# Performance work log

Measured on AMD Instinct MI355X. Metric: run time of the kernel, lower is better.

The kernel has to match this reference:

```python
import jax, jax.numpy as jnp
import numpy as np

B, S, F = 16, 511, 128           # batch, input seq len, n_features
D, H, NB = 512, 8, 6             # embedding_dim, n_heads, n_blocks
DH = D // H                      # d_head
MLP = 4 * D                      # mlp_ratio=4 hard-coded in FxtBlock
OUT = 1                          # out_d
T = S + 1                        # tokens incl. cls
EPS = 1e-5                       # torch LayerNorm default eps


def pos_emb(seq_len, d):
    # matches get_positional_embeddings: sin for even j, cos for odd j (with j-1 exponent)
    i = np.arange(seq_len, dtype=np.float32)[:, None]
    j = np.arange(d)
    je = np.where(j % 2 == 0, j, j - 1).astype(np.float32)
    ang = i / (10000.0 ** (je / d))
    pe = np.where(j % 2 == 0, np.sin(ang), np.cos(ang))
    return jnp.asarray(pe, jnp.float32)


def layernorm(x, g, b):
    m = jnp.mean(x, axis=-1, keepdims=True)
    v = jnp.mean((x - m) ** 2, axis=-1, keepdims=True)
    return (x - m) * jax.lax.rsqrt(v + EPS) * g + b


def setup_inputs() -> dict:
    key = jax.random.key(0)
    ks = jax.random.split(key, 12)
    g = lambda k, shape: jax.random.normal(k, shape, jnp.float32) * 0.02
    return {
        "src": jax.random.normal(ks[0], (B, S, F), jnp.float32),
        "emb_W": g(ks[1], (F, D)), "emb_b": jnp.zeros((D,), jnp.float32),
        "cls_tok": jax.random.uniform(ks[2], (1, D), jnp.float32),
        "ln1_g": jnp.ones((NB, D), jnp.float32), "ln1_b": jnp.zeros((NB, D), jnp.float32),
        "Wq": g(ks[3], (NB, H, DH, DH)), "bq": jnp.zeros((NB, H, DH), jnp.float32),
        "Wk": g(ks[4], (NB, H, DH, DH)), "bk": jnp.zeros((NB, H, DH), jnp.float32),
        "Wv": g(ks[5], (NB, H, DH, DH)), "bv": jnp.zeros((NB, H, DH), jnp.float32),
        "ln2_g": jnp.ones((NB, D), jnp.float32), "ln2_b": jnp.zeros((NB, D), jnp.float32),
        "W1": g(ks[6], (NB, D, MLP)), "b1": jnp.zeros((NB, MLP), jnp.float32),
        "W2": g(ks[7], (NB, MLP, D)), "b2": jnp.zeros((NB, D), jnp.float32),
        "head_W": g(ks[8], (D, OUT)), "head_b": jnp.zeros((OUT,), jnp.float32),
    }


def reference(src, emb_W, emb_b, cls_tok, ln1_g, ln1_b, Wq, bq, Wk, bk, Wv, bv,
              ln2_g, ln2_b, W1, b1, W2, b2, head_W, head_b):
    b = src.shape[0]
    x = src @ emb_W + emb_b                                    # [B,S,D]
    cls = jnp.broadcast_to(cls_tok[None], (b, 1, D))
    x = jnp.concatenate([cls, x], axis=1) + pos_emb(T, D)[None]  # [B,T,D]
    scale = 1.0 / jnp.sqrt(jnp.float32(DH))
    for i in range(NB):
        h = layernorm(x, ln1_g[i], ln1_b[i])
        hh = h.reshape(b, T, H, DH)
        q = jnp.einsum('bthd,hde->bhte', hh, Wq[i]) + bq[i][None, :, None, :]
        k = jnp.einsum('bthd,hde->bhte', hh, Wk[i]) + bk[i][None, :, None, :]
        v = jnp.einsum('bthd,hde->bhte', hh, Wv[i]) + bv[i][None, :, None, :]
        attn = jax.nn.softmax(jnp.einsum('bhse,bhte->bhst', q, k) * scale, axis=-1)
        o = jnp.einsum('bhst,bhte->bhse', attn, v)             # [B,H,T,DH]
        x = x + o.transpose(0, 2, 1, 3).reshape(b, T, D)
        h2 = layernorm(x, ln2_g[i], ln2_b[i])
        x = x + (jax.nn.gelu(h2 @ W1[i] + b1[i], approximate=False) @ W2[i] + b2[i])
    return jax.nn.sigmoid(x[:, 0] @ head_W + head_b)           # [B,OUT]
```

## Files before the change

### kernel.cpp

```cpp
#include <hip/hip_runtime.h>
#include <hip/hip_bf16.h>
#include <math.h>

#define B 16
#define S 511
#define F 128
#define D 512
#define H 8
#define NB 6
#define DH 64
#define MLPD 2048
#define T 512
#define EPS 1e-5f

typedef unsigned short ushort;
typedef __attribute__((ext_vector_type(8))) short short8;
typedef __attribute__((ext_vector_type(4))) float floatx4;

__device__ __forceinline__ ushort f2bf(float f) {
    union { float f; unsigned u; } cv; cv.f = f;
    unsigned r = (cv.u + 0x7fff + ((cv.u >> 16) & 1)) >> 16;
    return (ushort)r;
}

__device__ __forceinline__ float fast_gelu(float x) {
    float z = fabsf(x) * 0.70710678118f;
    float t = 1.0f / (1.0f + 0.3275911f * z);
    float p = ((((1.061405429f * t - 1.453152027f) * t + 1.421413741f) * t
               - 0.284496736f) * t + 0.254829592f) * t;
    float erfv = 1.0f - p * __expf(-z * z);
    erfv = copysignf(erfv, x);
    return 0.5f * x * (1.0f + erfv);
}

__global__ void castsrc_kernel(const float* __restrict__ src, ushort* __restrict__ srcb) {
    int row = blockIdx.x;
    int t = row & (T - 1), b = row >> 9;
    int tid = threadIdx.x;
    ushort v = 0;
    if (t > 0) v = f2bf(src[((size_t)b * S + (t - 1)) * F + tid]);
    srcb[(size_t)row * F + tid] = v;
}

__global__ void wtrans_kernel(const float* __restrict__ W,
                              ushort* __restrict__ Wt,
                              int K, int N) {
    int kb = blockIdx.x * 32, nb = blockIdx.y * 32, mat = blockIdx.z;
    __shared__ float tile[32][33];
    int tid = threadIdx.x;
    int c = tid & 31, r0 = tid >> 5;
    const float* Wm = W + (size_t)mat * K * N;
    ushort* Wtm = Wt + (size_t)mat * K * N;
    #pragma unroll
    for (int l = 0; l < 4; ++l) {
        int r = r0 + l * 8;
        tile[r][c] = Wm[(size_t)(kb + r) * N + nb + c];
    }
    __syncthreads();
    #pragma unroll
    for (int l = 0; l < 4; ++l) {
        int r = r0 + l * 8;
        Wtm[(size_t)(nb + r) * K + kb + c] = f2bf(tile[c][r]);
    }
}

__global__ void wtransq_kernel(const float* __restrict__ Wq, const float* __restrict__ Wk,
                               const float* __restrict__ Wv,
                               ushort* __restrict__ WqT, ushort* __restrict__ WkT,
                               ushort* __restrict__ WvT) {
    int mat = blockIdx.x;
    int which = blockIdx.y;
    const float* W = (which == 0 ? Wq : which == 1 ? Wk : Wv) + (size_t)mat * 4096;
    ushort* O = (which == 0 ? WqT : which == 1 ? WkT : WvT) + (size_t)mat * 4096;
    __shared__ float t[64][65];
    int tid = threadIdx.x;
    int r0 = tid >> 6, c = tid & 63;
    #pragma unroll
    for (int l = 0; l < 16; ++l) {
        int row = r0 * 16 + l;
        t[row][c] = W[row * 64 + c];
    }
    __syncthreads();
    #pragma unroll
    for (int l = 0; l < 16; ++l) {
        int row = r0 * 16 + l;
        O[row * 64 + c] = f2bf(t[c][row]);
    }
}

__device__ __forceinline__ void gload_lds16(const ushort* g, ushort* l) {
    __builtin_amdgcn_global_load_lds((const __attribute__((address_space(1))) unsigned int*)g,
                                     (__attribute__((address_space(3))) unsigned int*)l,
                                     16, 0, 0);
}

#define S_WAITCNT_VM(N) asm volatile("s_waitcnt vmcnt(" #N ")" ::: "memory")
#define S_WAITCNT_LGKM0 asm volatile("s_waitcnt lgkmcnt(0)" ::: "memory")

__global__ __launch_bounds__(256) void embed_gemm(const ushort* __restrict__ A,
                                                  const ushort* __restrict__ Bt,
                                                  const float* __restrict__ emb_b,
                                                  const float* __restrict__ cls_tok,
                                                  float* __restrict__ x) {
    __shared__ ushort As[64 * 32];
    __shared__ ushort Bs[64 * 32];
    int tid = threadIdx.x;
    int lane = tid & 63;
    int w = __builtin_amdgcn_readfirstlane(tid >> 6);
    int quad = lane >> 4, l15 = lane & 15;
    int wr = (w >> 1) * 32, wc = (w & 1) * 32;
    int m0 = blockIdx.x * 64, n0 = blockIdx.y * 64;

    floatx4 acc[2][2];
    #pragma unroll
    for (int i = 0; i < 2; ++i)
        #pragma unroll
        for (int j = 0; j < 2; ++j) acc[i][j] = (floatx4)0.f;

    int lrow = lane >> 2;
    int lk = (lane & 3) * 8;
    const ushort* Ag = A + (size_t)(m0 + 16 * w + lrow) * F + lk;
    const ushort* Bg = Bt + (size_t)(n0 + 16 * w + lrow) * F + lk;
    ushort* AsW = &As[16 * w * 32];
    ushort* BsW = &Bs[16 * w * 32];
    int fa = l15 * 32 + quad * 8;

    for (int kt = 0; kt < F; kt += 32) {
        gload_lds16(Ag + kt, AsW);
        gload_lds16(Bg + kt, BsW);
        __syncthreads();
        short8 af[2], bf[2];
        #pragma unroll
        for (int i = 0; i < 2; ++i) af[i] = *(const short8*)&As[(wr + 16 * i) * 32 + fa];
        #pragma unroll
        for (int j = 0; j < 2; ++j) bf[j] = *(const short8*)&Bs[(wc + 16 * j) * 32 + fa];
        #pragma unroll
        for (int i = 0; i < 2; ++i)
            #pragma unroll
            for (int j = 0; j < 2; ++j)
                acc[i][j] = __builtin_amdgcn_mfma_f32_16x16x32_bf16(af[i], bf[j], acc[i][j], 0, 0, 0);
        __syncthreads();
    }

    const float LOG1E4 = 9.210340371976184f;
    int rbase = (lane >> 4) * 4;
    int cidx = lane & 15;
    #pragma unroll
    for (int j = 0; j < 2; ++j) {
        int gc = n0 + wc + 16 * j + cidx;
        float je = (float)(gc & ~1);
        float freq = expf(-(je / (float)D) * LOG1E4);
        float ebv = emb_b[gc];
        float clsv = cls_tok[gc];
        bool odd = (gc & 1);
        #pragma unroll
        for (int i = 0; i < 2; ++i) {
            int gr = m0 + wr + 16 * i + rbase;
            #pragma unroll
            for (int reg = 0; reg < 4; ++reg) {
                int row = gr + reg;
                int t = row & (T - 1);
                float ang = (float)t * freq;
                float pe = odd ? cosf(ang) : sinf(ang);
                float val = (t == 0) ? (clsv + pe) : (acc[i][j][reg] + ebv + pe);
                x[(size_t)row * D + gc] = val;
            }
        }
    }
}

__global__ __launch_bounds__(256) void ln_kernel(const float* __restrict__ xin,
                                                 const float* __restrict__ g,
                                                 const float* __restrict__ bb,
                                                 ushort* __restrict__ out) {
    int lane = threadIdx.x & 63;
    int row = blockIdx.x * 4 + (threadIdx.x >> 6);
    const float* xr = xin + (size_t)row * D + lane * 8;
    float4 a0 = *(const float4*)xr;
    float4 a1 = *(const float4*)(xr + 4);
    float s = a0.x + a0.y + a0.z + a0.w + a1.x + a1.y + a1.z + a1.w;
    #pragma unroll
    for (int off = 1; off < 64; off <<= 1) s += __shfl_xor(s, off);
    float mean = s * (1.0f / (float)D);
    float d0 = a0.x - mean, d1 = a0.y - mean, d2 = a0.z - mean, d3 = a0.w - mean;
    float d4 = a1.x - mean, d5 = a1.y - mean, d6 = a1.z - mean, d7 = a1.w - mean;
    float sq = d0*d0 + d1*d1 + d2*d2 + d3*d3 + d4*d4 + d5*d5 + d6*d6 + d7*d7;
    #pragma unroll
    for (int off = 1; off < 64; off <<= 1) sq += __shfl_xor(sq, off);
    float rstd = rsqrtf(sq * (1.0f / (float)D) + EPS);
    const float* gp = g + lane * 8;
    const float* bp = bb + lane * 8;
    float4 g0 = *(const float4*)gp, g1 = *(const float4*)(gp + 4);
    float4 b0 = *(const float4*)bp, b1 = *(const float4*)(bp + 4);
    short8 o;
    o[0] = (short)f2bf(d0 * rstd * g0.x + b0.x);
    o[1] = (short)f2bf(d1 * rstd * g0.y + b0.y);
    o[2] = (short)f2bf(d2 * rstd * g0.z + b0.z);
    o[3] = (short)f2bf(d3 * rstd * g0.w + b0.w);
    o[4] = (short)f2bf(d4 * rstd * g1.x + b1.x);
    o[5] = (short)f2bf(d5 * rstd * g1.y + b1.y);
    o[6] = (short)f2bf(d6 * rstd * g1.z + b1.z);
    o[7] = (short)f2bf(d7 * rstd * g1.w + b1.w);
    *(short8*)(out + (size_t)row * D + lane * 8) = o;
}

__global__ __launch_bounds__(256) void ln_fuse_kernel(float* __restrict__ x,
                                                      const float* __restrict__ p0,
                                                      const float* __restrict__ g,
                                                      const float* __restrict__ bb,
                                                      ushort* __restrict__ out) {
    int lane = threadIdx.x & 63;
    int row = blockIdx.x * 4 + (threadIdx.x >> 6);
    size_t base = (size_t)row * D + lane * 8;
    float* xr = x + base;
    float4 a0 = *(const float4*)xr;
    float4 a1 = *(const float4*)(xr + 4);
    float4 q0 = *(const float4*)(p0 + base);
    float4 q1 = *(const float4*)(p0 + base + 4);
    a0.x += q0.x; a0.y += q0.y; a0.z += q0.z; a0.w += q0.w;
    a1.x += q1.x; a1.y += q1.y; a1.z += q1.z; a1.w += q1.w;
    *(float4*)xr = a0;
    *(float4*)(xr + 4) = a1;
    float s = a0.x + a0.y + a0.z + a0.w + a1.x + a1.y + a1.z + a1.w;
    #pragma unroll
    for (int off = 1; off < 64; off <<= 1) s += __shfl_xor(s, off);
    float mean = s * (1.0f / (float)D);
    float d0 = a0.x - mean, d1 = a0.y - mean, d2 = a0.z - mean, d3 = a0.w - mean;
    float d4 = a1.x - mean, d5 = a1.y - mean, d6 = a1.z - mean, d7 = a1.w - mean;
    float sq = d0*d0 + d1*d1 + d2*d2 + d3*d3 + d4*d4 + d5*d5 + d6*d6 + d7*d7;
    #pragma unroll
    for (int off = 1; off < 64; off <<= 1) sq += __shfl_xor(sq, off);
    float rstd = rsqrtf(sq * (1.0f / (float)D) + EPS);
    const float* gp = g + lane * 8;
    const float* bp = bb + lane * 8;
    float4 g0 = *(const float4*)gp, g1 = *(const float4*)(gp + 4);
    float4 b0 = *(const float4*)bp, b1 = *(const float4*)(bp + 4);
    short8 o;
    o[0] = (short)f2bf(d0 * rstd * g0.x + b0.x);
    o[1] = (short)f2bf(d1 * rstd * g0.y + b0.y);
    o[2] = (short)f2bf(d2 * rstd * g0.z + b0.z);
    o[3] = (short)f2bf(d3 * rstd * g0.w + b0.w);
    o[4] = (short)f2bf(d4 * rstd * g1.x + b1.x);
    o[5] = (short)f2bf(d5 * rstd * g1.y + b1.y);
    o[6] = (short)f2bf(d6 * rstd * g1.z + b1.z);
    o[7] = (short)f2bf(d7 * rstd * g1.w + b1.w);
    *(short8*)(out + (size_t)row * D + lane * 8) = o;
}

__global__ __launch_bounds__(256) void qkv_kernel(
        const ushort* __restrict__ hb,
        const ushort* __restrict__ WqT, const float* __restrict__ bq,
        const ushort* __restrict__ WkT, const float* __restrict__ bk,
        const ushort* __restrict__ WvT, const float* __restrict__ bv,
        ushort* __restrict__ qo, ushort* __restrict__ ko, ushort* __restrict__ vTo) {
    int m0 = blockIdx.x * 128;
    int hh = blockIdx.y;
    int tid = threadIdx.x;
    int lane = tid & 63;
    int w = __builtin_amdgcn_readfirstlane(tid >> 6);
    int quad = lane >> 4, l15 = lane & 15;

    short8 af[2][2];
    #pragma unroll
    for (int mt = 0; mt < 2; ++mt) {
        const ushort* ab = hb + (size_t)(m0 + w * 32 + mt * 16 + l15) * D + hh * DH + quad * 8;
        af[mt][0] = *(const short8*)(ab);
        af[mt][1] = *(const short8*)(ab + 32);
    }

    floatx4 acc[3][2][4];
    #pragma unroll
    for (int xo = 0; xo < 3; ++xo)
        #pragma unroll
        for (int mt = 0; mt < 2; ++mt)
            #pragma unroll
            for (int nt = 0; nt < 4; ++nt) acc[xo][mt][nt] = (floatx4)0.f;

    #pragma unroll
    for (int xo = 0; xo < 3; ++xo) {
        const ushort* WT = (xo == 0 ? WqT : xo == 1 ? WkT : WvT) + (size_t)hh * 4096;
        #pragma unroll
        for (int nt = 0; nt < 4; ++nt) {
            const ushort* wb = WT + (size_t)(nt * 16 + l15) * 64 + quad * 8;
            short8 bf0 = *(const short8*)(wb);
            short8 bf1 = *(const short8*)(wb + 32);
            #pragma unroll
            for (int mt = 0; mt < 2; ++mt) {
                acc[xo][mt][nt] = __builtin_amdgcn_mfma_f32_16x16x32_bf16(af[mt][0], bf0, acc[xo][mt][nt], 0, 0, 0);
                acc[xo][mt][nt] = __builtin_amdgcn_mfma_f32_16x16x32_bf16(af[mt][1], bf1, acc[xo][mt][nt], 0, 0, 0);
            }
        }
    }

    int bb = m0 >> 9;
    int bh = bb * H + hh;
    #pragma unroll
    for (int mt = 0; mt < 2; ++mt) {
        int trow = m0 + w * 32 + mt * 16 + quad * 4;
        int tt = trow & (T - 1);
        #pragma unroll
        for (int nt = 0; nt < 4; ++nt) {
            int col = nt * 16 + l15;
            float bqv = bq[hh * DH + col];
            float bkv = bk[hh * DH + col];
            float bvv = bv[hh * DH + col];
            #pragma unroll
            for (int reg = 0; reg < 4; ++reg) {
                qo[((size_t)bh * T + tt + reg) * DH + col] = f2bf(acc[0][mt][nt][reg] + bqv);
                ko[((size_t)bh * T + tt + reg) * DH + col] = f2bf(acc[1][mt][nt][reg] + bkv);
                vTo[((size_t)bh * DH + col) * T + tt + reg] = f2bf(acc[2][mt][nt][reg] + bvv);
            }
        }
    }
}

#define PSTRIDE 88
__global__ __launch_bounds__(256) void attn_kernel(const ushort* __restrict__ q,
                                                   const ushort* __restrict__ k,
                                                   const ushort* __restrict__ vT,
                                                   float* __restrict__ x) {
    int bh = blockIdx.x;
    int qt = blockIdx.y;
    int b = bh >> 3, hh = bh & 7;
    int tid = threadIdx.x;
    int lane = tid & 63;
    int w = __builtin_amdgcn_readfirstlane(tid >> 6);
    int quad = lane >> 4, l15 = lane & 15;

    __shared__ __align__(16) ushort smem[22016];
    ushort* Pw = smem + 16384 + w * (16 * PSTRIDE);

    const ushort* qbase = q + ((size_t)bh * T + qt * 64 + w * 16 + l15) * DH + quad * 8;
    short8 Qf0 = *(const short8*)(qbase);
    short8 Qf1 = *(const short8*)(qbase + 32);

    const ushort* kbase = k + (size_t)bh * T * DH;
    const ushort* vbase = vT + (size_t)bh * DH * T;

    int srow = lane >> 2;
    int scol = (lane & 3) * 8;
    const ushort* kg = kbase + (size_t)(w * 16 + srow) * DH + scol;
    const ushort* vg = vbase + (size_t)(w * 16 + srow) * T + scol;
    ushort* ldsK = smem + w * 16 * 32;
    ushort* ldsV = smem + 8192 + w * 16 * 32;

    float l_i[4] = {0.f, 0.f, 0.f, 0.f};
    floatx4 O[4];
    #pragma unroll
    for (int j = 0; j < 4; ++j) O[j] = (floatx4)0.f;

    gload_lds16(kg, ldsK);
    gload_lds16(kg + 32, ldsK + 2048);
    gload_lds16(vg, ldsV);
    gload_lds16(vg + 32, ldsV + 2048);
    __syncthreads();

    for (int kt = 0; kt < T / 64; ++kt) {
        int cur = kt & 1;
        if (kt < T / 64 - 1) {
            int nb = cur ^ 1;
            const ushort* kgn = kg + (size_t)(kt + 1) * 64 * DH;
            const ushort* vgn = vg + (kt + 1) * 64;
            gload_lds16(kgn, ldsK + nb * 4096);
            gload_lds16(kgn + 32, ldsK + nb * 4096 + 2048);
            gload_lds16(vgn, ldsV + nb * 4096);
            gload_lds16(vgn + 32, ldsV + nb * 4096 + 2048);
        }
        const ushort* Kc = smem + cur * 4096;
        const ushort* Vc = smem + 8192 + cur * 4096;

        floatx4 sc[4];
        #pragma unroll
        for (int j = 0; j < 4; ++j) {
            int ro = (j * 16 + l15) * 32 + quad * 8;
            short8 kf0 = *(const short8*)&Kc[ro];
            short8 kf1 = *(const short8*)&Kc[2048 + ro];
            floatx4 s4 = (floatx4)0.f;
            s4 = __builtin_amdgcn_mfma_f32_16x16x32_bf16(Qf0, kf0, s4, 0, 0, 0);
            s4 = __builtin_amdgcn_mfma_f32_16x16x32_bf16(Qf1, kf1, s4, 0, 0, 0);
            sc[j] = s4;
        }
        #pragma unroll
        for (int j = 0; j < 4; ++j) {
            #pragma unroll
            for (int r = 0; r < 4; ++r) {
                float p = __expf(sc[j][r] * 0.125f);
                ushort pb = f2bf(p);
                union { unsigned u; float f; } cv; cv.u = ((unsigned)pb) << 16;
                l_i[r] += cv.f;
                Pw[(quad * 4 + r) * PSTRIDE + j * 16 + l15] = pb;
            }
        }

        short8 af0 = *(const short8*)&Pw[l15 * PSTRIDE + quad * 8];
        short8 af1 = *(const short8*)&Pw[l15 * PSTRIDE + 32 + quad * 8];
        #pragma unroll
        for (int j = 0; j < 4; ++j) {
            int ro = (j * 16 + l15) * 32 + quad * 8;
            short8 vf0 = *(const short8*)&Vc[ro];
            short8 vf1 = *(const short8*)&Vc[2048 + ro];
            O[j] = __builtin_amdgcn_mfma_f32_16x16x32_bf16(af0, vf0, O[j], 0, 0, 0);
            O[j] = __builtin_amdgcn_mfma_f32_16x16x32_bf16(af1, vf1, O[j], 0, 0, 0);
        }
        __syncthreads();
    }

    #pragma unroll
    for (int r = 0; r < 4; ++r) {
        l_i[r] += __shfl_xor(l_i[r], 1);
        l_i[r] += __shfl_xor(l_i[r], 2);
        l_i[r] += __shfl_xor(l_i[r], 4);
        l_i[r] += __shfl_xor(l_i[r], 8);
    }

    float* Ow = (float*)smem + w * 16 * 68;
    #pragma unroll
    for (int r = 0; r < 4; ++r) {
        float rl = 1.0f / l_i[r];
        #pragma unroll
        for (int j = 0; j < 4; ++j)
            Ow[(quad * 4 + r) * 68 + j * 16 + l15] = O[j][r] * rl;
    }
    __syncthreads();
    int r4 = lane >> 4;
    int c16 = lane & 15;
    #pragma unroll
    for (int i = 0; i < 4; ++i) {
        int lrow = i * 4 + r4;
        float4 o = *(const float4*)&Ow[lrow * 68 + c16 * 4];
        int grow = qt * 64 + w * 16 + lrow;
        float* xp = &x[((size_t)(b * T) + grow) * D + hh * DH + c16 * 4];
        float4 xv = *(const float4*)xp;
        xv.x += o.x; xv.y += o.y; xv.z += o.z; xv.w += o.w;
        *(float4*)xp = xv;
    }
}

__global__ __launch_bounds__(512, 2) void gemm1_8ph(const ushort* __restrict__ A,
                                                    const ushort* __restrict__ Bt,
                                                    const float* __restrict__ bias,
                                                    ushort* __restrict__ C,
                                                    int N, int K) {
    constexpr int BK = 64;
    constexpr int BUF = 32768;
    constexpr int BOF = 16384;
    __shared__ ushort lds[2 * BUF];

    int tid = threadIdx.x;
    int lane = tid & 63;
    int w = __builtin_amdgcn_readfirstlane(tid >> 6);
    int quad = lane >> 4, l15 = lane & 15;
    int wm = w >> 2, wn = w & 3;
    int wmr = wm * 128, wnr = wn * 64;

    int nwg = gridDim.x;
    int id = blockIdx.x;
    int idx = (id & 7) * (nwg >> 3) + (id >> 3);
    int NTg = N >> 8;
    int mt = idx / NTg, nt = idx - mt * NTg;
    int m0 = mt * 256, n0 = nt * 256;

    int rr = tid >> 3;
    int scol = ((tid & 7) ^ (rr & 7)) * 8;
    const ushort* AgS = A + (size_t)(m0 + rr) * K + scol;
    const ushort* BgS = Bt + (size_t)(n0 + rr) * K + scol;
    int woff = (w * 8) * BK;

    int sx0 = (quad ^ (l15 & 7)) * 8;
    int sx1 = ((4 + quad) ^ (l15 & 7)) * 8;

    floatx4 acc[8][4];
    #pragma unroll
    for (int i = 0; i < 8; ++i)
        #pragma unroll
        for (int n = 0; n < 4; ++n) acc[i][n] = (floatx4)0.f;

    short8 a[4][2], b[4][2];

    #define STG_A(th, h, bb) do {                                                          \
        gload_lds16(AgS + (size_t)((h) * 128) * K + (size_t)(th) * BK,                     \
                    (bb) + ((h) * 128) * BK + woff);                                       \
        gload_lds16(AgS + (size_t)((h) * 128 + 64) * K + (size_t)(th) * BK,                \
                    (bb) + ((h) * 128 + 64) * BK + woff);                                  \
    } while (0)
    #define STG_B(th, h, bb) do {                                                          \
        gload_lds16(BgS + (size_t)((h) * 128) * K + (size_t)(th) * BK,                     \
                    (bb) + BOF + ((h) * 128) * BK + woff);                                 \
        gload_lds16(BgS + (size_t)((h) * 128 + 64) * K + (size_t)(th) * BK,                \
                    (bb) + BOF + ((h) * 128 + 64) * BK + woff);                            \
    } while (0)

    #define MFMA_Q(mb, nb2) do {                                                           \
        _Pragma("unroll")                                                                  \
        for (int ks = 0; ks < 2; ++ks)                                                     \
            _Pragma("unroll")                                                              \
            for (int i = 0; i < 4; ++i)                                                    \
                _Pragma("unroll")                                                          \
                for (int n = 0; n < 2; ++n)                                                \
                    acc[(mb) + i][(nb2) + n] = __builtin_amdgcn_mfma_f32_16x16x32_bf16(    \
                        a[i][ks], b[(nb2) + n][ks], acc[(mb) + i][(nb2) + n], 0, 0, 0);    \
    } while (0)

    STG_A(0, 0, lds); STG_A(0, 1, lds); STG_B(0, 0, lds); STG_B(0, 1, lds);
    STG_A(1, 0, lds + BUF);

    int NT = K >> 6;
    for (int t = 0; t < NT; ++t) {
        ushort* bufc = lds + (t & 1) * BUF;
        ushort* bufn = lds + (((t & 1) ^ 1)) * BUF;
        bool sn = (t + 1 < NT);
        if (t == NT - 1) { S_WAITCNT_VM(0); } else { S_WAITCNT_VM(2); }
        __builtin_amdgcn_s_barrier();
        #pragma unroll
        for (int ks = 0; ks < 2; ++ks) {
            int sx = ks ? sx1 : sx0;
            #pragma unroll
            for (int i = 0; i < 4; ++i)
                a[i][ks] = *(const short8*)&bufc[(wmr + i * 16 + l15) * BK + sx];
            #pragma unroll
            for (int n = 0; n < 2; ++n)
                b[n][ks] = *(const short8*)&bufc[BOF + (wnr + n * 16 + l15) * BK + sx];
        }
        if (sn) STG_A(t + 1, 1, bufn);
        S_WAITCNT_LGKM0;
        __builtin_amdgcn_s_setprio(1);
        MFMA_Q(0, 0);
        __builtin_amdgcn_s_setprio(0);
        #pragma unroll
        for (int ks = 0; ks < 2; ++ks) {
            int sx = ks ? sx1 : sx0;
            #pragma unroll
            for (int n = 0; n < 2; ++n)
                b[2 + n][ks] = *(const short8*)&bufc[BOF + (wnr + (2 + n) * 16 + l15) * BK + sx];
        }
        if (sn) STG_B(t + 1, 0, bufn);
        S_WAITCNT_LGKM0;
        __builtin_amdgcn_s_setprio(1);
        MFMA_Q(0, 2);
        __builtin_amdgcn_s_setprio(0);
        #pragma unroll
        for (int ks = 0; ks < 2; ++ks) {
            int sx = ks ? sx1 : sx0;
            #pragma unroll
            for (int i = 0; i < 4; ++i)
                a[i][ks] = *(const short8*)&bufc[(wmr + (4 + i) * 16 + l15) * BK + sx];
        }
        if (sn) STG_B(t + 1, 1, bufn);
        S_WAITCNT_LGKM0;
        __builtin_amdgcn_s_setprio(1);
        MFMA_Q(4, 2);
        __builtin_amdgcn_s_setprio(0);
        __builtin_amdgcn_s_barrier();
        if (t + 2 < NT) STG_A(t + 2, 0, bufc);
        __builtin_amdgcn_s_setprio(1);
        MFMA_Q(4, 0);
        __builtin_amdgcn_s_setprio(0);
    }

    #undef STG_A
    #undef STG_B
    #undef MFMA_Q

    int rbase = quad * 4;
    #pragma unroll
    for (int i = 0; i < 8; ++i) {
        #pragma unroll
        for (int n = 0; n < 4; ++n) {
            int gc = n0 + wnr + n * 16 + l15;
            float bv = bias[gc];
            int gr = m0 + wmr + i * 16 + rbase;
            #pragma unroll
            for (int reg = 0; reg < 4; ++reg) {
                C[(size_t)(gr + reg) * N + gc] = f2bf(fast_gelu(acc[i][n][reg] + bv));
            }
        }
    }
}

__global__ __launch_bounds__(256, 2) void gemm_db(const ushort* __restrict__ A,
                                                  const ushort* __restrict__ Bt,
                                                  const float* __restrict__ bias,
                                                  float* __restrict__ Cout,
                                                  int N, int K) {
    constexpr int BK = 64;
    __shared__ ushort lds0[256 * BK];
    __shared__ ushort lds1[256 * BK];

    int tid = threadIdx.x;
    int lane = tid & 63;
    int w = __builtin_amdgcn_readfirstlane(tid >> 6);
    int quad = lane >> 4, l15 = lane & 15;
    int wrow = (w >> 1) * 64;
    int wcol = (w & 1) * 64;

    int nwg = gridDim.x;
    int id = blockIdx.x;
    int idx = (id & 7) * (nwg >> 3) + (id >> 3);
    int NTg = N >> 7;
    int mt = idx / NTg;
    int nt = idx - mt * NTg;
    int m0 = mt * 128, n0 = nt * 128;

    int lrow = tid >> 3;
    int lslot = tid & 7;
    int scol = (lslot ^ (lrow & 7)) * 8;
    const ushort* Asrc = A + (size_t)(m0 + lrow) * K + scol;
    const ushort* Bsrc = Bt + (size_t)(n0 + lrow) * K + scol;
    int ldsAoff = (w * 8) * BK;
    int ldsBoff = 128 * BK + (w * 8) * BK;

    int sx0 = ((quad) ^ (l15 & 7)) * 8;
    int sx1 = ((4 + quad) ^ (l15 & 7)) * 8;

    floatx4 acc[4][4];
    #pragma unroll
    for (int i = 0; i < 4; ++i)
        #pragma unroll
        for (int n = 0; n < 4; ++n) acc[i][n] = (floatx4)0.f;

    #define STAGE(t, Lb) do {                                                     \
        const ushort* ap_ = Asrc + (size_t)(t) * BK;                              \
        const ushort* bp_ = Bsrc + (size_t)(t) * BK;                              \
        _Pragma("unroll")                                                         \
        for (int j = 0; j < 4; ++j)                                               \
            gload_lds16(ap_ + (size_t)j * 32 * K, (Lb) + ldsAoff + j * 32 * BK);  \
        _Pragma("unroll")                                                         \
        for (int j = 0; j < 4; ++j)                                               \
            gload_lds16(bp_ + (size_t)j * 32 * K, (Lb) + ldsBoff + j * 32 * BK);  \
    } while (0)

    #define COMP(Lb) do {                                                         \
        const ushort* Ab_ = (Lb);                                                 \
        const ushort* Bb_ = (Lb) + 128 * BK;                                      \
        _Pragma("unroll")                                                         \
        for (int ks = 0; ks < 2; ++ks) {                                          \
            int sx_ = ks ? sx1 : sx0;                                             \
            short8 bfr[4];                                                        \
            _Pragma("unroll")                                                     \
            for (int n = 0; n < 4; ++n)                                           \
                bfr[n] = *(const short8*)&Bb_[(wcol + n * 16 + l15) * BK + sx_];  \
            _Pragma("unroll")                                                     \
            for (int i = 0; i < 4; ++i) {                                         \
                short8 af_ = *(const short8*)&Ab_[(wrow + i * 16 + l15) * BK + sx_]; \
                _Pragma("unroll")                                                 \
                for (int n = 0; n < 4; ++n)                                       \
                    acc[i][n] = __builtin_amdgcn_mfma_f32_16x16x32_bf16(af_, bfr[n], acc[i][n], 0, 0, 0); \
            }                                                                     \
        }                                                                         \
    } while (0)

    int NT = K >> 6;
    STAGE(0, lds0);
    for (int t = 0; t < NT - 2; t += 2) {
        STAGE(t + 1, lds1);
        S_WAITCNT_VM(8);
        __builtin_amdgcn_s_barrier();
        __builtin_amdgcn_s_setprio(1);
        COMP(lds0);
        __builtin_amdgcn_s_setprio(0);
        S_WAITCNT_LGKM0;
        __builtin_amdgcn_s_barrier();
        STAGE(t + 2, lds0);
        S_WAITCNT_VM(8);
        __builtin_amdgcn_s_barrier();
        __builtin_amdgcn_s_setprio(1);
        COMP(lds1);
        __builtin_amdgcn_s_setprio(0);
        S_WAITCNT_LGKM0;
        __builtin_amdgcn_s_barrier();
    }
    STAGE(NT - 1, lds1);
    S_WAITCNT_VM(8);
    __builtin_amdgcn_s_barrier();
    __builtin_amdgcn_s_setprio(1);
    COMP(lds0);
    __builtin_amdgcn_s_setprio(0);
    S_WAITCNT_LGKM0;
    __builtin_amdgcn_s_barrier();
    S_WAITCNT_VM(0);
    __builtin_amdgcn_s_barrier();
    COMP(lds1);

    #undef STAGE
    #undef COMP

    int rbase = quad * 4;
    #pragma unroll
    for (int i = 0; i < 4; ++i) {
        #pragma unroll
        for (int n = 0; n < 4; ++n) {
            int gc = n0 + wcol + n * 16 + l15;
            float bv = bias[gc];
            int gr = m0 + wrow + i * 16 + rbase;
            #pragma unroll
            for (int reg = 0; reg < 4; ++reg) {
                Cout[(size_t)(gr + reg) * N + gc] = acc[i][n][reg] + bv;
            }
        }
    }
}

__global__ void head_kernel(const float* __restrict__ x,
                            const float* __restrict__ p0,
                            const float* __restrict__ hw,
                            const float* __restrict__ hb,
                            float* __restrict__ out) {
    int b = blockIdx.x;
    int tid = threadIdx.x;
    size_t idx = (size_t)b * T * D + tid;
    float s = (x[idx] + p0[idx]) * hw[tid];
    #pragma unroll
    for (int off = 32; off > 0; off >>= 1) s += __shfl_down(s, off, 64);
    __shared__ float red[8];
    if ((tid & 63) == 0) red[tid >> 6] = s;
    __syncthreads();
    if (tid == 0) {
        float t = 0.f;
        #pragma unroll
        for (int i = 0; i < 8; ++i) t += red[i];
        out[b] = 1.0f / (1.0f + __expf(-(t + hb[0])));
    }
}

extern "C" void kernel_launch(void* const* d_in, const int* in_sizes, int n_in,
                              void* d_out, int out_size, void* d_ws, size_t ws_size,
                              hipStream_t stream) {
    const float* src     = (const float*)d_in[0];
    const float* emb_W   = (const float*)d_in[1];
    const float* emb_b   = (const float*)d_in[2];
    const float* cls_tok = (const float*)d_in[3];
    const float* ln1_g   = (const float*)d_in[4];
    const float* ln1_b   = (const float*)d_in[5];
    const float* Wq      = (const float*)d_in[6];
    const float* bq      = (const float*)d_in[7];
    const float* Wk      = (const float*)d_in[8];
    const float* bk      = (const float*)d_in[9];
    const float* Wv      = (const float*)d_in[10];
    const float* bv      = (const float*)d_in[11];
    const float* ln2_g   = (const float*)d_in[12];
    const float* ln2_b   = (const float*)d_in[13];
    const float* W1      = (const float*)d_in[14];
    const float* b1      = (const float*)d_in[15];
    const float* W2      = (const float*)d_in[16];
    const float* b2      = (const float*)d_in[17];
    const float* head_W  = (const float*)d_in[18];
    const float* head_b  = (const float*)d_in[19];

    const size_t NTOK = (size_t)B * T;
    char* wsb = (char*)d_ws;
    float*  x    = (float*)wsb;      wsb += NTOK * D * 4;
    float*  p0   = (float*)wsb;      wsb += NTOK * D * 4;
    ushort* hbuf = (ushort*)wsb;     wsb += NTOK * D * 2;
    ushort* q    = (ushort*)wsb;     wsb += NTOK * D * 2;
    ushort* k    = (ushort*)wsb;     wsb += NTOK * D * 2;
    ushort* vT   = (ushort*)wsb;     wsb += NTOK * D * 2;
    ushort* u    = (ushort*)wsb;     wsb += NTOK * MLPD * 2;
    ushort* W1t  = (ushort*)wsb;     wsb += (size_t)NB * D * MLPD * 2;
    ushort* W2t  = (ushort*)wsb;     wsb += (size_t)NB * D * MLPD * 2;
    ushort* WqT  = (ushort*)wsb;     wsb += (size_t)NB * H * DH * DH * 2;
    ushort* WkT  = (ushort*)wsb;     wsb += (size_t)NB * H * DH * DH * 2;
    ushort* WvT  = (ushort*)wsb;     wsb += (size_t)NB * H * DH * DH * 2;
    ushort* srcb = (ushort*)wsb;     wsb += NTOK * F * 2;
    ushort* embWt= (ushort*)wsb;     wsb += (size_t)F * D * 2;

    wtrans_kernel<<<dim3(D / 32, MLPD / 32, NB), 256, 0, stream>>>(W1, W1t, D, MLPD);
    wtrans_kernel<<<dim3(MLPD / 32, D / 32, NB), 256, 0, stream>>>(W2, W2t, MLPD, D);
    wtransq_kernel<<<dim3(NB * H, 3), 256, 0, stream>>>(Wq, Wk, Wv, WqT, WkT, WvT);
    wtrans_kernel<<<dim3(F / 32, D / 32, 1), 256, 0, stream>>>(emb_W, embWt, F, D);
    castsrc_kernel<<<B * T, F, 0, stream>>>(src, srcb);

    embed_gemm<<<dim3(B * T / 64, D / 64), 256, 0, stream>>>(srcb, embWt, emb_b, cls_tok, x);

    for (int i = 0; i < NB; ++i) {
        if (i == 0)
            ln_kernel<<<B * T / 4, 256, 0, stream>>>(x, ln1_g, ln1_b, hbuf);
        else
            ln_fuse_kernel<<<B * T / 4, 256, 0, stream>>>(x, p0,
                ln1_g + i * D, ln1_b + i * D, hbuf);
        qkv_kernel<<<dim3(B * T / 128, H), 256, 0, stream>>>(hbuf,
            WqT + (size_t)i * H * DH * DH, bq + (size_t)i * H * DH,
            WkT + (size_t)i * H * DH * DH, bk + (size_t)i * H * DH,
            WvT + (size_t)i * H * DH * DH, bv + (size_t)i * H * DH,
            q, k, vT);
        attn_kernel<<<dim3(B * H, T / 64), 256, 0, stream>>>(q, k, vT, x);
        ln_kernel<<<B * T / 4, 256, 0, stream>>>(x, ln2_g + i * D, ln2_b + i * D, hbuf);
        gemm1_8ph<<<dim3((B * T / 256) * (MLPD / 256)), 512, 0, stream>>>(
            hbuf, W1t + (size_t)i * D * MLPD, b1 + (size_t)i * MLPD, u, MLPD, D);
        gemm_db<<<dim3((B * T / 128) * (D / 128)), 256, 0, stream>>>(
            u, W2t + (size_t)i * MLPD * D, b2 + (size_t)i * D, p0, D, MLPD);
    }

    head_kernel<<<B, 512, 0, stream>>>(x, p0, head_W, head_b, (float*)d_out);
}
```

Before: 837.6 us.

## Restructure second MLP GEMM into four-phase interleaved load/MFMA pipeline

Replaces the double-buffered second MLP GEMM with a schedule that splits each K-tile's compute into four quadrant MFMA groups. Global-to-LDS loads for the next tile are issued in halves between those groups, so memory traffic overlaps with matrix math at a finer grain. Fewer fragments are held in registers at once. The attention kernel also now accumulates the softmax denominator from the fp32 probability rather than the bf16-rounded value, which drops a conversion but slightly changes numerics. The new schedule relies on careful waitcnt and barrier placement, so any ordering mistake risks races.

```diff
diff --git a/kernel.cpp b/kernel.cpp
--- a/kernel.cpp
+++ b/kernel.cpp
@@ -385,10 +385,8 @@
             #pragma unroll
             for (int r = 0; r < 4; ++r) {
                 float p = __expf(sc[j][r] * 0.125f);
-                ushort pb = f2bf(p);
-                union { unsigned u; float f; } cv; cv.u = ((unsigned)pb) << 16;
-                l_i[r] += cv.f;
-                Pw[(quad * 4 + r) * PSTRIDE + j * 16 + l15] = pb;
+                l_i[r] += p;
+                Pw[(quad * 4 + r) * PSTRIDE + j * 16 + l15] = f2bf(p);
             }
         }
 
@@ -577,14 +575,15 @@
     }
 }
 
-__global__ __launch_bounds__(256, 2) void gemm_db(const ushort* __restrict__ A,
-                                                  const ushort* __restrict__ Bt,
-                                                  const float* __restrict__ bias,
-                                                  float* __restrict__ Cout,
-                                                  int N, int K) {
+__global__ __launch_bounds__(256, 2) void gemm2_4ph(const ushort* __restrict__ A,
+                                                    const ushort* __restrict__ Bt,
+                                                    const float* __restrict__ bias,
+                                                    float* __restrict__ Cout,
+                                                    int N, int K) {
     constexpr int BK = 64;
-    __shared__ ushort lds0[256 * BK];
-    __shared__ ushort lds1[256 * BK];
+    constexpr int BUF = 16384;
+    constexpr int BOF = 8192;
+    __shared__ ushort lds[2 * BUF];
 
     int tid = threadIdx.x;
     int lane = tid & 63;
@@ -597,19 +596,16 @@
     int id = blockIdx.x;
     int idx = (id & 7) * (nwg >> 3) + (id >> 3);
     int NTg = N >> 7;
-    int mt = idx / NTg;
-    int nt = idx - mt * NTg;
+    int mt = idx / NTg, nt = idx - mt * NTg;
     int m0 = mt * 128, n0 = nt * 128;
 
-    int lrow = tid >> 3;
-    int lslot = tid & 7;
-    int scol = (lslot ^ (lrow & 7)) * 8;
-    const ushort* Asrc = A + (size_t)(m0 + lrow) * K + scol;
-    const ushort* Bsrc = Bt + (size_t)(n0 + lrow) * K + scol;
-    int ldsAoff = (w * 8) * BK;
-    int ldsBoff = 128 * BK + (w * 8) * BK;
-
-    int sx0 = ((quad) ^ (l15 & 7)) * 8;
+    int rr = tid >> 3;
+    int scol = ((tid & 7) ^ (rr & 7)) * 8;
+    const ushort* AgS = A + (size_t)(m0 + rr) * K + scol;
+    const ushort* BgS = Bt + (size_t)(n0 + rr) * K + scol;
+    int woff = (w * 8) * BK;
+
+    int sx0 = (quad ^ (l15 & 7)) * 8;
     int sx1 = ((4 + quad) ^ (l15 & 7)) * 8;
 
     floatx4 acc[4][4];
@@ -618,71 +614,91 @@
         #pragma unroll
         for (int n = 0; n < 4; ++n) acc[i][n] = (floatx4)0.f;
 
-    #define STAGE(t, Lb) do {                                                     \
-        const ushort* ap_ = Asrc + (size_t)(t) * BK;                              \
-        const ushort* bp_ = Bsrc + (size_t)(t) * BK;                              \
-        _Pragma("unroll")                                                         \
-        for (int j = 0; j < 4; ++j)                                               \
-            gload_lds16(ap_ + (size_t)j * 32 * K, (Lb) + ldsAoff + j * 32 * BK);  \
-        _Pragma("unroll")                                                         \
-        for (int j = 0; j < 4; ++j)                                               \
-            gload_lds16(bp_ + (size_t)j * 32 * K, (Lb) + ldsBoff + j * 32 * BK);  \
+    short8 a2[2][2], b2[4][2];
+
+    #define STG2_A(th, h, bb) do {                                                         \
+        gload_lds16(AgS + (size_t)((h) * 64) * K + (size_t)(th) * BK,                      \
+                    (bb) + ((h) * 64) * BK + woff);                                        \
+        gload_lds16(AgS + (size_t)((h) * 64 + 32) * K + (size_t)(th) * BK,                 \
+                    (bb) + ((h) * 64 + 32) * BK + woff);                                   \
     } while (0)
-
-    #define COMP(Lb) do {                                                         \
-        const ushort* Ab_ = (Lb);                                                 \
-        const ushort* Bb_ = (Lb) + 128 * BK;                                      \
-        _Pragma("unroll")                                                         \
-        for (int ks = 0; ks < 2; ++ks) {                                          \
-            int sx_ = ks ? sx1 : sx0;                                             \
-            short8 bfr[4];                                                        \
-            _Pragma("unroll")                                                     \
-            for (int n = 0; n < 4; ++n)                                           \
-                bfr[n] = *(const short8*)&Bb_[(wcol + n * 16 + l15) * BK + sx_];  \
-            _Pragma("unroll")                                                     \
-            for (int i = 0; i < 4; ++i) {                                         \
-                short8 af_ = *(const short8*)&Ab_[(wrow + i * 16 + l15) * BK + sx_]; \
-                _Pragma("unroll")                                                 \
-                for (int n = 0; n < 4; ++n)                                       \
-                    acc[i][n] = __builtin_amdgcn_mfma_f32_16x16x32_bf16(af_, bfr[n], acc[i][n], 0, 0, 0); \
-            }                                                                     \
-        }                                                                         \
+    #define STG2_B(th, h, bb) do {                                                         \
+        gload_lds16(BgS + (size_t)((h) * 64) * K + (size_t)(th) * BK,                      \
+                    (bb) + BOF + ((h) * 64) * BK + woff);                                  \
+        gload_lds16(BgS + (size_t)((h) * 64 + 32) * K + (size_t)(th) * BK,                 \
+                    (bb) + BOF + ((h) * 64 + 32) * BK + woff);                             \
     } while (0)
 
+    #define MFMA_Q2(mb, nb2) do {                                                          \
+        _Pragma("unroll")                                                                  \
+        for (int ks = 0; ks < 2; ++ks)                                                     \
+            _Pragma("unroll")                                                              \
+            for (int i = 0; i < 2; ++i)                                                    \
+                _Pragma("unroll")                                                          \
+                for (int n = 0; n < 2; ++n)                                                \
+                    acc[(mb) + i][(nb2) + n] = __builtin_amdgcn_mfma_f32_16x16x32_bf16(    \
+                        a2[i][ks], b2[(nb2) + n][ks], acc[(mb) + i][(nb2) + n], 0, 0, 0);  \
+    } while (0)
+
+    STG2_A(0, 0, lds); STG2_A(0, 1, lds); STG2_B(0, 0, lds); STG2_B(0, 1, lds);
+    STG2_A(1, 0, lds + BUF);
+
     int NT = K >> 6;
-    STAGE(0, lds0);
-    for (int t = 0; t < NT - 2; t += 2) {
-        STAGE(t + 1, lds1);
-        S_WAITCNT_VM(8);
+    for (int t = 0; t < NT; ++t) {
+        ushort* bufc = lds + (t & 1) * BUF;
+        ushort* bufn = lds + (((t & 1) ^ 1)) * BUF;
+        bool sn = (t + 1 < NT);
+        if (t == NT - 1) { S_WAITCNT_VM(0); } else { S_WAITCNT_VM(2); }
         __builtin_amdgcn_s_barrier();
+        #pragma unroll
+        for (int ks = 0; ks < 2; ++ks) {
+            int sx = ks ? sx1 : sx0;
+            #pragma unroll
+            for (int i = 0; i < 2; ++i)
+                a2[i][ks] = *(const short8*)&bufc[(wrow + i * 16 + l15) * BK + sx];
+            #pragma unroll
+            for (int n = 0; n < 2; ++n)
+                b2[n][ks] = *(const short8*)&bufc[BOF + (wcol + n * 16 + l15) * BK + sx];
+        }
+        if (sn) STG2_A(t + 1, 1, bufn);
+        S_WAITCNT_LGKM0;
         __builtin_amdgcn_s_setprio(1);
-        COMP(lds0);
+        MFMA_Q2(0, 0);
         __builtin_amdgcn_s_setprio(0);
+        #pragma unroll
+        for (int ks = 0; ks < 2; ++ks) {
+            int sx = ks ? sx1 : sx0;
+            #pragma unroll
+            for (int n = 0; n < 2; ++n)
+                b2[2 + n][ks] = *(const short8*)&bufc[BOF + (wcol + (2 + n) * 16 + l15) * BK + sx];
+        }
+        if (sn) STG2_B(t + 1, 0, bufn);
         S_WAITCNT_LGKM0;
+        __builtin_amdgcn_s_setprio(1);
+        MFMA_Q2(0, 2);
+        __builtin_amdgcn_s_setprio(0);
+        #pragma unroll
+        for (int ks = 0; ks < 2; ++ks) {
+            int sx = ks ? sx1 : sx0;
+            #pragma unroll
+            for (int i = 0; i < 2; ++i)
+                a2[i][ks] = *(const short8*)&bufc[(wrow + (2 + i) * 16 + l15) * BK + sx];
+        }
+        if (sn) STG2_B(t + 1, 1, bufn);
+        S_WAITCNT_LGKM0;
+        __builtin_amdgcn_s_setprio(1);
+        MFMA_Q2(2, 2);
+        __builtin_amdgcn_s_setprio(0);
         __builtin_amdgcn_s_barrier();
-        STAGE(t + 2, lds0);
-        S_WAITCNT_VM(8);
-        __builtin_amdgcn_s_barrier();
+        if (t + 2 < NT) STG2_A(t + 2, 0, bufc);
         __builtin_amdgcn_s_setprio(1);
-        COMP(lds1);
+        MFMA_Q2(2, 0);
         __builtin_amdgcn_s_setprio(0);
-        S_WAITCNT_LGKM0;
-        __builtin_amdgcn_s_barrier();
-    }
-    STAGE(NT - 1, lds1);
-    S_WAITCNT_VM(8);
-    __builtin_amdgcn_s_barrier();
-    __builtin_amdgcn_s_setprio(1);
-    COMP(lds0);
-    __builtin_amdgcn_s_setprio(0);
-    S_WAITCNT_LGKM0;
-    __builtin_amdgcn_s_barrier();
-    S_WAITCNT_VM(0);
-    __builtin_amdgcn_s_barrier();
-    COMP(lds1);
-
-    #undef STAGE
-    #undef COMP
+    }
+
+    #undef STG2_A
+    #undef STG2_B
+    #undef MFMA_Q2
 
     int rbase = quad * 4;
     #pragma unroll
@@ -786,7 +802,7 @@
         ln_kernel<<<B * T / 4, 256, 0, stream>>>(x, ln2_g + i * D, ln2_b + i * D, hbuf);
         gemm1_8ph<<<dim3((B * T / 256) * (MLPD / 256)), 512, 0, stream>>>(
             hbuf, W1t + (size_t)i * D * MLPD, b1 + (size_t)i * MLPD, u, MLPD, D);
-        gemm_db<<<dim3((B * T / 128) * (D / 128)), 256, 0, stream>>>(
+        gemm2_4ph<<<dim3((B * T / 128) * (D / 128)), 256, 0, stream>>>(
             u, W2t + (size_t)i * MLPD * D, b2 + (size_t)i * D, p0, D, MLPD);
     }
 
```

Measured after the change: 845.5 us. About the same (+0.9%).
